# Kernel optimization log

Hardware: AMD Instinct MI355X
Metric: run time of the kernel (lower is better)

## Reference

```python
import jax, jax.numpy as jnp
import numpy as np

N_NODES = 100000
N_EDGES = 1600000
IN_CH = 32
HID = 128
EDGE_DIM = 16
BN_EPS = 1e-5


def setup_inputs() -> dict:
    key = jax.random.key(0)
    ks = jax.random.split(key, 32)
    f32 = jnp.float32

    def w(k, shape, scale):
        return jax.random.normal(k, shape, dtype=f32) * scale

    inp = {
        'x': w(ks[0], (N_NODES, IN_CH), 1.0),
        'edge_index': jax.random.randint(ks[1], (2, N_EDGES), 0, N_NODES, dtype=jnp.int32),
        'edge_attr': w(ks[2], (N_EDGES, EDGE_DIM), 1.0),
        # layer 0: in=32 -> out=128
        'l0_We': w(ks[3], (EDGE_DIM, IN_CH), 0.1),
        'l0_be': jnp.zeros((IN_CH,), f32),
        'l0_W1': w(ks[4], (IN_CH, HID), 0.1),
        'l0_b1': jnp.zeros((HID,), f32),
        'l0_W2': w(ks[5], (HID, HID), 0.1),
        'l0_b2': jnp.zeros((HID,), f32),
        'l0_gamma': jnp.ones((HID,), f32),
        'l0_beta': jnp.zeros((HID,), f32),
        # layer 1: 128 -> 128
        'l1_We': w(ks[6], (EDGE_DIM, HID), 0.1),
        'l1_be': jnp.zeros((HID,), f32),
        'l1_W1': w(ks[7], (HID, HID), 0.1),
        'l1_b1': jnp.zeros((HID,), f32),
        'l1_W2': w(ks[8], (HID, HID), 0.1),
        'l1_b2': jnp.zeros((HID,), f32),
        'l1_gamma': jnp.ones((HID,), f32),
        'l1_beta': jnp.zeros((HID,), f32),
        # head MLP: hidden -> hidden -> 1
        'head_W1': w(ks[9], (HID, HID), 0.1),
        'head_b1': jnp.zeros((HID,), f32),
        'head_W2': w(ks[10], (HID, 1), 0.1),
        'head_b2': jnp.zeros((1,), f32),
    }
    return inp


def _gnblock(x, src, dst, e, We, be, W1, b1, W2, b2, gamma, beta):
    # GINE-style message passing: gather -> edge message -> scatter-sum
    msg = jax.nn.relu(x[src] + e @ We + be)              # [E, d_in]
    agg = jax.ops.segment_sum(msg, dst, num_segments=N_NODES)  # [N, d_in]
    h = x + agg                                          # GIN combine (eps=0)
    h = jax.nn.relu(h @ W1 + b1) @ W2 + b2               # 2-layer MLP
    # batch norm over the node dimension (use_norm=True)
    mu = jnp.mean(h, axis=0)
    var = jnp.var(h, axis=0)
    h = (h - mu) * jax.lax.rsqrt(var + BN_EPS) * gamma + beta
    return jax.nn.relu(h)


def reference(x, edge_index, edge_attr,
              l0_We, l0_be, l0_W1, l0_b1, l0_W2, l0_b2, l0_gamma, l0_beta,
              l1_We, l1_be, l1_W1, l1_b1, l1_W2, l1_b2, l1_gamma, l1_beta,
              head_W1, head_b1, head_W2, head_b2):
    src, dst = edge_index[0], edge_index[1]
    h = _gnblock(x, src, dst, edge_attr,
                 l0_We, l0_be, l0_W1, l0_b1, l0_W2, l0_b2, l0_gamma, l0_beta)
    h = _gnblock(h, src, dst, edge_attr,
                 l1_We, l1_be, l1_W1, l1_b1, l1_W2, l1_b2, l1_gamma, l1_beta)
    # MLPBlock head + sigmoid -> per-node selection probability [N, 1]
    out = jax.nn.relu(h @ head_W1 + head_b1) @ head_W2 + head_b2
    return jax.nn.sigmoid(out)
```

## Files before the change

kernel.cpp:

```cpp
#include <hip/hip_runtime.h>

#define NN 100000
#define NE 1600000
#define TMAX 193760
#define NRANGES 24220

typedef unsigned int uint32;
typedef unsigned long long ull;
typedef __attribute__((ext_vector_type(8))) short bf16x8;
typedef __attribute__((ext_vector_type(4))) float f32x4;

__device__ __forceinline__ unsigned short f2bf(float f) {
  unsigned int u = __float_as_uint(f);
  unsigned int r = (u + 0x7fffu + ((u >> 16) & 1u)) >> 16;
  return (unsigned short)r;
}
__device__ __forceinline__ float bf2f(unsigned short u) {
  return __uint_as_float(((unsigned int)u) << 16);
}
__device__ __forceinline__ unsigned int pack2(float a, float b) {
  return (unsigned int)f2bf(a) | ((unsigned int)f2bf(b) << 16);
}
__device__ __forceinline__ uint32 pack2ru(float a, float b) {
  const uint32 ua = __float_as_uint(a) + 0x8000u;
  const uint32 ub = __float_as_uint(b) + 0x8000u;
  return (ua >> 16) | (ub & 0xffff0000u);
}
__device__ __forceinline__ float row16_sum(float x) {
  x += __int_as_float(__builtin_amdgcn_mov_dpp(__float_as_int(x), 0x128, 0xf, 0xf, false));
  x += __int_as_float(__builtin_amdgcn_mov_dpp(__float_as_int(x), 0x124, 0xf, 0xf, false));
  x += __int_as_float(__builtin_amdgcn_mov_dpp(__float_as_int(x), 0x122, 0xf, 0xf, false));
  x += __int_as_float(__builtin_amdgcn_mov_dpp(__float_as_int(x), 0x121, 0xf, 0xf, false));
  return x;
}

__device__ __forceinline__ void wconv_body(const float* __restrict__ src,
    unsigned short* __restrict__ dst, int K, int N, int b)
{
  const int i = b * 256 + threadIdx.x;
  if (i < K * N) {
    const int n = i / K, k = i - n * K;
    dst[i] = f2bf(src[k * N + n]);
  }
}

__global__ __launch_bounds__(256) void conv_all(
    const float* __restrict__ l0W1, const float* __restrict__ l0W2,
    const float* __restrict__ l1W1, const float* __restrict__ l1W2,
    const float* __restrict__ hW1,  const float* __restrict__ l0We,
    const float* __restrict__ l1We, const float* __restrict__ x,
    unsigned short* __restrict__ W1t0, unsigned short* __restrict__ W2t0,
    unsigned short* __restrict__ W1t1, unsigned short* __restrict__ W2t1,
    unsigned short* __restrict__ hW1t, unsigned short* __restrict__ Wet0,
    unsigned short* __restrict__ Wet1, unsigned short* __restrict__ xb)
{
  int b = blockIdx.x;
  if (b < 16)  { wconv_body(l0W1, W1t0, 32, 128, b); return; }  b -= 16;
  if (b < 64)  { wconv_body(l0W2, W2t0, 128, 128, b); return; } b -= 64;
  if (b < 64)  { wconv_body(l1W1, W1t1, 128, 128, b); return; } b -= 64;
  if (b < 64)  { wconv_body(l1W2, W2t1, 128, 128, b); return; } b -= 64;
  if (b < 64)  { wconv_body(hW1,  hW1t, 128, 128, b); return; } b -= 64;
  if (b < 2)   { wconv_body(l0We, Wet0, 16, 32, b); return; }   b -= 2;
  if (b < 8)   { wconv_body(l1We, Wet1, 16, 128, b); return; }  b -= 8;
  const int i = b * 256 + threadIdx.x;
  if (i * 8 < NN * 32) {
    const float4 a = ((const float4*)x)[i * 2];
    const float4 d = ((const float4*)x)[i * 2 + 1];
    uint4 o;
    o.x = pack2(a.x, a.y); o.y = pack2(a.z, a.w);
    o.z = pack2(d.x, d.y); o.w = pack2(d.z, d.w);
    ((uint4*)xb)[i] = o;
  }
}

__global__ __launch_bounds__(256) void hist_kernel(
    const int* __restrict__ ei, uint32* __restrict__ deg)
{
  const int e = blockIdx.x * 256 + threadIdx.x;
  if (e < NE) atomicAdd(&deg[ei[NE + e]], 1u);
}

__global__ __launch_bounds__(256) void offsets2_kernel(
    const uint32* __restrict__ deg, uint32* __restrict__ toff,
    uint32* __restrict__ eoff, ull* __restrict__ counter)
{
  __shared__ ull s[256];
  __shared__ ull base;
  const int tid = threadIdx.x;
  const int n = blockIdx.x * 256 + tid;
  const uint32 d = (n < NN) ? deg[n] : 0u;
  const uint32 tc = (d + 15u) >> 4;
  const ull v = ((ull)tc << 32) | (ull)d;
  s[tid] = v;
  __syncthreads();
#pragma unroll
  for (int st = 1; st < 256; st <<= 1) {
    ull w = (tid >= st) ? s[tid - st] : 0ull;
    __syncthreads();
    s[tid] += w;
    __syncthreads();
  }
  if (tid == 255) base = atomicAdd(counter, s[255]);
  __syncthreads();
  if (n < NN) {
    const ull t = base + (s[tid] - v);
    toff[n] = (uint32)(t >> 32);
    eoff[n] = (uint32)t;
  }
}

__global__ __launch_bounds__(256) void snode_fill(
    const uint32* __restrict__ toff, const uint32* __restrict__ deg,
    int* __restrict__ snode)
{
  const int n = blockIdx.x * 256 + threadIdx.x;
  if (n < NN) {
    const uint32 t0 = toff[n];
    const uint32 tc = (deg[n] + 15u) >> 4;
    for (uint32 i = 0; i < tc; ++i) snode[t0 + i] = n;
  }
}

__global__ __launch_bounds__(256) void fill_kernel(
    const int* __restrict__ ei, const uint32* __restrict__ eoff,
    uint32* __restrict__ cnt, uint2* __restrict__ esrc2)
{
  const int e = blockIdx.x * 256 + threadIdx.x;
  if (e < NE) {
    const int dst = ei[NE + e];
    const uint32 pos = eoff[dst] + atomicAdd(&cnt[dst], 1u);
    esrc2[pos] = make_uint2((uint32)e, (uint32)ei[e]);
  }
}

template<int D, int NCT>
__global__ __launch_bounds__(256) void flat_agg3(
    const int* __restrict__ snode, const uint32* __restrict__ toff,
    const uint32* __restrict__ eoff, const uint32* __restrict__ deg,
    const uint2* __restrict__ esrc2, const float* __restrict__ ea,
    const unsigned short* __restrict__ hsrc,
    const unsigned short* __restrict__ Wet, const float* __restrict__ be,
    const ull* __restrict__ tot, float* __restrict__ agg)
{
  const int tid = threadIdx.x;
  const int wid = tid >> 6;
  const int lane = tid & 63;
  const int c = lane & 15;
  const int g = lane >> 4;
  constexpr bool HALF = (NCT * 16 != D);
  int range, ch0;
  if (HALF) { range = blockIdx.x * 2 + (wid >> 1); ch0 = (wid & 1) * (NCT * 16); }
  else      { range = blockIdx.x * 4 + wid;        ch0 = 0; }
  const int tile0 = range * 8;
  const uint32 ntile = (uint32)((*tot) >> 32);
  if ((uint32)tile0 >= ntile) return;

  bf16x8 wf[NCT];
#pragma unroll
  for (int ct = 0; ct < NCT; ++ct) {
    const int chA = ch0 + (c >> 2) * (NCT * 4) + ct * 4 + (c & 3);
    uint4 u = make_uint4(0u, 0u, 0u, 0u);
    if (g < 2) u = *(const uint4*)&Wet[chA * 16 + g * 8];
    else if (g == 2) u.x = (0xFE96u << 16) | (uint32)f2bf(be[chA]);
    union { uint4 u4; bf16x8 v; } cv; cv.u4 = u;
    wf[ct] = cv.v;
  }

  int sn8 = -1, pk8 = 0, p_ = 0;
  if (lane < 8) {
    sn8 = snode[tile0 + lane];
    if (sn8 >= 0) {
      const uint32 to = toff[sn8], dg = deg[sn8], eo = eoff[sn8];
      const int k = tile0 + lane - (int)to;
      p_ = (int)eo + k * 16;
      int rv = (int)dg - k * 16; if (rv > 16) rv = 16;
      const int fl = (k == 0 ? 1 : 0) |
                     ((k == (int)((dg + 15u) >> 4) - 1) ? 2 : 0);
      pk8 = (rv << 7) | (fl << 12);
    }
  }
  const int p0base = __shfl(p_, 0);
  if (lane < 8 && sn8 >= 0) pk8 |= (p_ - p0base);

  const uint2 q0 = esrc2[(size_t)p0base + lane];
  const uint2 q1 = esrc2[(size_t)p0base + 64 + lane];

  float acc[NCT][4];
#pragma unroll
  for (int ct = 0; ct < NCT; ++ct) {
    acc[ct][0] = 0.f; acc[ct][1] = 0.f; acc[ct][2] = 0.f; acc[ct][3] = 0.f;
  }
  int openNode = -1; bool openFull = false, openClosed = false;

  auto flushOpen = [&](bool storeOK) {
#pragma unroll
    for (int ct = 0; ct < NCT; ++ct)
#pragma unroll
      for (int j = 0; j < 4; ++j)
        acc[ct][j] = row16_sum(acc[ct][j]);
    float4 sv = make_float4(0.f, 0.f, 0.f, 0.f);
#pragma unroll
    for (int ct = 0; ct < NCT; ++ct)
      if (c == ct)
        sv = make_float4(acc[ct][0], acc[ct][1], acc[ct][2], acc[ct][3]);
    if (c < NCT) {
      float* p = &agg[(size_t)openNode * D + ch0 + g * (NCT * 4) + c * 4];
      if (storeOK) {
        *(float4*)p = sv;
      } else {
        atomicAdd(p + 0, sv.x); atomicAdd(p + 1, sv.y);
        atomicAdd(p + 2, sv.z); atomicAdd(p + 3, sv.w);
      }
    }
  };

  auto issue = [&](int t, float4& E0, float4& E1, uint4& h0, uint4& h1,
                   int& n_, int& mt_) {
    n_ = __shfl(sn8, t);
    mt_ = __shfl(pk8, t);
    const int d0 = mt_ & 127;
    const int rem = (mt_ >> 7) & 31;
    const int idx = d0 + ((c < rem) ? c : 0);
    const int li = idx & 63;
    const uint32 eA = (uint32)__shfl((int)q0.x, li);
    const uint32 eB = (uint32)__shfl((int)q1.x, li);
    const uint32 sA = (uint32)__shfl((int)q0.y, li);
    const uint32 sB = (uint32)__shfl((int)q1.y, li);
    const int e   = (int)((idx & 64) ? eB : eA);
    const int src = (int)((idx & 64) ? sB : sA);
    if (g < 2) {
      E0 = *(const float4*)&ea[(size_t)e * 16 + g * 8];
      E1 = *(const float4*)&ea[(size_t)e * 16 + g * 8 + 4];
    }
    h0 = *(const uint4*)&hsrc[(size_t)src * D + ch0 + g * (NCT * 4)];
    if constexpr (NCT == 4)
      h1 = *(const uint4*)&hsrc[(size_t)src * D + ch0 + g * (NCT * 4) + 8];
  };

  auto compute = [&](const float4 E0, const float4 E1, const uint4 h0,
                     const uint4 h1, const int n, const int mt) {
    if (n < 0) return;
    const int rem = (mt >> 7) & 31;
    const int fl = mt >> 12;
    if (n != openNode) {
      if (openNode >= 0) {
        flushOpen(openFull);
#pragma unroll
        for (int ct = 0; ct < NCT; ++ct) {
          acc[ct][0] = 0.f; acc[ct][1] = 0.f;
          acc[ct][2] = 0.f; acc[ct][3] = 0.f;
        }
      }
      openNode = n; openFull = (fl & 1) != 0; openClosed = false;
    }
    if (fl & 2) openClosed = true;
    bf16x8 afv;
    {
      uint4 u = make_uint4(0u, 0u, 0u, 0u);
      if (g < 2) {
        u.x = pack2ru(E0.x, E0.y); u.y = pack2ru(E0.z, E0.w);
        u.z = pack2ru(E1.x, E1.y); u.w = pack2ru(E1.z, E1.w);
      } else if (g == 2) {
        u.x = (c < rem) ? 0x3f80u : 0x3f803f80u;
      }
      union { uint4 u4; bf16x8 v; } cv; cv.u4 = u; afv = cv.v;
    }
#pragma unroll
    for (int ct = 0; ct < NCT; ++ct) {
      f32x4 pre = __builtin_amdgcn_mfma_f32_16x16x32_bf16(
          wf[ct], afv, (f32x4){0.f, 0.f, 0.f, 0.f}, 0, 0, 0);
#pragma unroll
      for (int j = 0; j < 4; ++j) {
        const int ix = ct * 4 + j;
        const uint4 hu = (ix < 8) ? h0 : h1;
        uint32 wv;
        switch ((ix & 7) >> 1) {
          case 0: wv = hu.x; break;
          case 1: wv = hu.y; break;
          case 2: wv = hu.z; break;
          default: wv = hu.w; break;
        }
        const float hvv = bf2f((unsigned short)((ix & 1) ? (wv >> 16) : (wv & 0xffffu)));
        acc[ct][j] += fmaxf(pre[j] + hvv, 0.f);
      }
    }
  };

  float4 eA0, eA1, eB0, eB1, eC0, eC1;
  uint4 h0A = make_uint4(0,0,0,0), h1A = make_uint4(0,0,0,0);
  uint4 h0B = make_uint4(0,0,0,0), h1B = make_uint4(0,0,0,0);
  uint4 h0C = make_uint4(0,0,0,0), h1C = make_uint4(0,0,0,0);
  int nA = -1, mA = 0, nB = -1, mB = 0, nC = -1, mC = 0;

  issue(0, eA0, eA1, h0A, h1A, nA, mA);
  issue(1, eB0, eB1, h0B, h1B, nB, mB);
  issue(2, eC0, eC1, h0C, h1C, nC, mC);
  compute(eA0, eA1, h0A, h1A, nA, mA); issue(3, eA0, eA1, h0A, h1A, nA, mA);
  compute(eB0, eB1, h0B, h1B, nB, mB); issue(4, eB0, eB1, h0B, h1B, nB, mB);
  compute(eC0, eC1, h0C, h1C, nC, mC); issue(5, eC0, eC1, h0C, h1C, nC, mC);
  compute(eA0, eA1, h0A, h1A, nA, mA); issue(6, eA0, eA1, h0A, h1A, nA, mA);
  compute(eB0, eB1, h0B, h1B, nB, mB); issue(7, eB0, eB1, h0B, h1B, nB, mB);
  compute(eC0, eC1, h0C, h1C, nC, mC);
  compute(eA0, eA1, h0A, h1A, nA, mA);
  compute(eB0, eB1, h0B, h1B, nB, mB);
  if (openNode >= 0) flushOpen(openFull && openClosed);
}

template<int DIN, bool ABF16>
__global__ __launch_bounds__(256) void mlp_mfma(
    const float* __restrict__ a32, const unsigned short* __restrict__ abf,
    const float* __restrict__ agg,
    const unsigned short* __restrict__ W1t, const float* __restrict__ b1,
    const unsigned short* __restrict__ W2t, const float* __restrict__ b2,
    float* __restrict__ outp, float* __restrict__ stats, int nChunks)
{
  constexpr int P1 = (DIN == 128) ? 136 : 40;
  constexpr int KS1 = DIN / 32;
  __shared__ __align__(16) unsigned short hin[64 * P1];
  __shared__ __align__(16) unsigned short tls[64 * 136];
  const int tid = threadIdx.x;
  const int w = tid >> 6;
  const int lane = tid & 63;
  const int c = lane & 15, g = lane >> 4;
  const int cw = w * 32;

  bf16x8 B1[2][KS1], B2[2][4];
#pragma unroll
  for (int ct = 0; ct < 2; ++ct)
#pragma unroll
    for (int kk = 0; kk < KS1; ++kk)
      B1[ct][kk] = *(const bf16x8*)&W1t[(cw + ct * 16 + c) * DIN + kk * 32 + g * 8];
#pragma unroll
  for (int ct = 0; ct < 2; ++ct)
#pragma unroll
    for (int kk = 0; kk < 4; ++kk)
      B2[ct][kk] = *(const bf16x8*)&W2t[(cw + ct * 16 + c) * 128 + kk * 32 + g * 8];
  const float b1c0 = b1[cw + c], b1c1 = b1[cw + 16 + c];
  const float b2c0 = b2[cw + c], b2c1 = b2[cw + 16 + c];
  float lsum0 = 0.f, lsum1 = 0.f, lsq0 = 0.f, lsq1 = 0.f;

  for (int chunk = blockIdx.x; chunk < nChunks; chunk += gridDim.x) {
    const int base = chunk * 64;
    if constexpr (DIN == 128) {
#pragma unroll
      for (int p = 0; p < 4; ++p) {
        const int idx = tid + 256 * p;
        const int n = idx >> 4, k8 = idx & 15;
        const int node = base + n;
        uint4 ov = make_uint4(0u, 0u, 0u, 0u);
        if (node < NN) {
          const float4 g0 = *(const float4*)&agg[node * 128 + k8 * 8];
          const float4 g1 = *(const float4*)&agg[node * 128 + k8 * 8 + 4];
          const uint4 hv = *(const uint4*)&abf[node * 128 + k8 * 8];
          ov.x = pack2(bf2f((unsigned short)(hv.x & 0xffffu)) + g0.x,
                       bf2f((unsigned short)(hv.x >> 16)) + g0.y);
          ov.y = pack2(bf2f((unsigned short)(hv.y & 0xffffu)) + g0.z,
                       bf2f((unsigned short)(hv.y >> 16)) + g0.w);
          ov.z = pack2(bf2f((unsigned short)(hv.z & 0xffffu)) + g1.x,
                       bf2f((unsigned short)(hv.z >> 16)) + g1.y);
          ov.w = pack2(bf2f((unsigned short)(hv.w & 0xffffu)) + g1.z,
                       bf2f((unsigned short)(hv.w >> 16)) + g1.w);
        }
        *(uint4*)&hin[n * P1 + k8 * 8] = ov;
      }
    } else {
      const int n = tid >> 2, k8 = tid & 3;
      const int node = base + n;
      uint4 ov = make_uint4(0u, 0u, 0u, 0u);
      if (node < NN) {
        const float4 x0 = *(const float4*)&a32[node * 32 + k8 * 8];
        const float4 x1 = *(const float4*)&a32[node * 32 + k8 * 8 + 4];
        const float4 g0 = *(const float4*)&agg[node * 32 + k8 * 8];
        const float4 g1 = *(const float4*)&agg[node * 32 + k8 * 8 + 4];
        ov.x = pack2(x0.x + g0.x, x0.y + g0.y);
        ov.y = pack2(x0.z + g0.z, x0.w + g0.w);
        ov.z = pack2(x1.x + g1.x, x1.y + g1.y);
        ov.w = pack2(x1.z + g1.z, x1.w + g1.w);
      }
      *(uint4*)&hin[n * P1 + k8 * 8] = ov;
    }
    __syncthreads();
#pragma unroll
    for (int nt = 0; nt < 4; ++nt) {
      bf16x8 af[KS1];
#pragma unroll
      for (int kk = 0; kk < KS1; ++kk)
        af[kk] = *(const bf16x8*)&hin[(nt * 16 + c) * P1 + kk * 32 + g * 8];
      f32x4 acc0 = {0.f, 0.f, 0.f, 0.f}, acc1 = {0.f, 0.f, 0.f, 0.f};
#pragma unroll
      for (int kk = 0; kk < KS1; ++kk) {
        acc0 = __builtin_amdgcn_mfma_f32_16x16x32_bf16(af[kk], B1[0][kk], acc0, 0, 0, 0);
        acc1 = __builtin_amdgcn_mfma_f32_16x16x32_bf16(af[kk], B1[1][kk], acc1, 0, 0, 0);
      }
#pragma unroll
      for (int j = 0; j < 4; ++j) {
        const int row = nt * 16 + g * 4 + j;
        tls[row * 136 + cw + c]      = f2bf(fmaxf(acc0[j] + b1c0, 0.f));
        tls[row * 136 + cw + 16 + c] = f2bf(fmaxf(acc1[j] + b1c1, 0.f));
      }
    }
    __syncthreads();
#pragma unroll
    for (int nt = 0; nt < 4; ++nt) {
      bf16x8 af[4];
#pragma unroll
      for (int kk = 0; kk < 4; ++kk)
        af[kk] = *(const bf16x8*)&tls[(nt * 16 + c) * 136 + kk * 32 + g * 8];
      f32x4 acc0 = {0.f, 0.f, 0.f, 0.f}, acc1 = {0.f, 0.f, 0.f, 0.f};
#pragma unroll
      for (int kk = 0; kk < 4; ++kk) {
        acc0 = __builtin_amdgcn_mfma_f32_16x16x32_bf16(af[kk], B2[0][kk], acc0, 0, 0, 0);
        acc1 = __builtin_amdgcn_mfma_f32_16x16x32_bf16(af[kk], B2[1][kk], acc1, 0, 0, 0);
      }
#pragma unroll
      for (int j = 0; j < 4; ++j) {
        const int node = base + nt * 16 + g * 4 + j;
        if (node < NN) {
          const float v0 = acc0[j] + b2c0;
          const float v1 = acc1[j] + b2c1;
          outp[node * 128 + cw + c] = v0;
          outp[node * 128 + cw + 16 + c] = v1;
          lsum0 += v0; lsq0 += v0 * v0;
          lsum1 += v1; lsq1 += v1 * v1;
        }
      }
    }
  }
  lsum0 += __shfl_xor(lsum0, 16); lsum0 += __shfl_xor(lsum0, 32);
  lsum1 += __shfl_xor(lsum1, 16); lsum1 += __shfl_xor(lsum1, 32);
  lsq0  += __shfl_xor(lsq0, 16);  lsq0  += __shfl_xor(lsq0, 32);
  lsq1  += __shfl_xor(lsq1, 16);  lsq1  += __shfl_xor(lsq1, 32);
  if (lane < 16) {
    atomicAdd(&stats[cw + lane], lsum0);
    atomicAdd(&stats[cw + 16 + lane], lsum1);
    atomicAdd(&stats[128 + cw + lane], lsq0);
    atomicAdd(&stats[128 + cw + 16 + lane], lsq1);
  }
}

__global__ void bn_finalize(float* __restrict__ stats,
                            const float* __restrict__ gamma,
                            const float* __restrict__ beta)
{
  const int cc = threadIdx.x;
  const float inv_n = 1.0f / (float)NN;
  const float mu = stats[cc] * inv_n;
  float var = stats[128 + cc] * inv_n - mu * mu;
  var = fmaxf(var, 0.f);
  const float rs = rsqrtf(var + 1e-5f);
  const float sc = rs * gamma[cc];
  stats[256 + cc] = sc;
  stats[384 + cc] = beta[cc] - mu * sc;
}

__global__ __launch_bounds__(256) void bn_apply_bf16(
    const float* __restrict__ h, const float* __restrict__ stats,
    unsigned short* __restrict__ hb)
{
  const int idx = blockIdx.x * 256 + threadIdx.x;
  const int c4 = (idx & 31) * 4;
  const float4 sc = *(const float4*)&stats[256 + c4];
  const float4 sh = *(const float4*)&stats[384 + c4];
  const float4 v = ((const float4*)h)[idx];
  const float r0 = fmaxf(fmaf(v.x, sc.x, sh.x), 0.f);
  const float r1 = fmaxf(fmaf(v.y, sc.y, sh.y), 0.f);
  const float r2 = fmaxf(fmaf(v.z, sc.z, sh.z), 0.f);
  const float r3 = fmaxf(fmaf(v.w, sc.w, sh.w), 0.f);
  uint2 o;
  o.x = pack2(r0, r1);
  o.y = pack2(r2, r3);
  ((uint2*)hb)[idx] = o;
}

__global__ __launch_bounds__(256) void head_bn(
    const float* __restrict__ hpre, const float* __restrict__ stats,
    const unsigned short* __restrict__ W1t, const float* __restrict__ b1,
    const float* __restrict__ w2, const float* __restrict__ b2,
    float* __restrict__ out, int nChunks)
{
  __shared__ float pl[4][64];
  const int tid = threadIdx.x;
  const int w = tid >> 6;
  const int lane = tid & 63;
  const int c = lane & 15, g = lane >> 4;
  const int cw = w * 32;

  bf16x8 B1[2][4];
#pragma unroll
  for (int ct = 0; ct < 2; ++ct)
#pragma unroll
    for (int kk = 0; kk < 4; ++kk)
      B1[ct][kk] = *(const bf16x8*)&W1t[(cw + ct * 16 + c) * 128 + kk * 32 + g * 8];
  const float b1c0 = b1[cw + c], b1c1 = b1[cw + 16 + c];
  const float w2c0 = w2[cw + c], w2c1 = w2[cw + 16 + c];
  const float b2v = b2[0];
  float4 scq[4][2], shq[4][2];
#pragma unroll
  for (int kk = 0; kk < 4; ++kk) {
    const int cb = kk * 32 + g * 8;
    scq[kk][0] = *(const float4*)&stats[256 + cb];
    scq[kk][1] = *(const float4*)&stats[256 + cb + 4];
    shq[kk][0] = *(const float4*)&stats[384 + cb];
    shq[kk][1] = *(const float4*)&stats[384 + cb + 4];
  }

  for (int chunk = blockIdx.x; chunk < nChunks; chunk += gridDim.x) {
    const int base = chunk * 64;
    float p[4][4];
#pragma unroll
    for (int nt = 0; nt < 4; ++nt) {
      const int node = base + nt * 16 + c;
      bf16x8 af[4];
#pragma unroll
      for (int kk = 0; kk < 4; ++kk) {
        uint4 u = make_uint4(0u, 0u, 0u, 0u);
        if (node < NN) {
          const float4 v0 = *(const float4*)&hpre[(size_t)node * 128 + kk * 32 + g * 8];
          const float4 v1 = *(const float4*)&hpre[(size_t)node * 128 + kk * 32 + g * 8 + 4];
          const float4 s0 = scq[kk][0], s1 = scq[kk][1];
          const float4 h0 = shq[kk][0], h1 = shq[kk][1];
          u.x = pack2(fmaxf(fmaf(v0.x, s0.x, h0.x), 0.f),
                      fmaxf(fmaf(v0.y, s0.y, h0.y), 0.f));
          u.y = pack2(fmaxf(fmaf(v0.z, s0.z, h0.z), 0.f),
                      fmaxf(fmaf(v0.w, s0.w, h0.w), 0.f));
          u.z = pack2(fmaxf(fmaf(v1.x, s1.x, h1.x), 0.f),
                      fmaxf(fmaf(v1.y, s1.y, h1.y), 0.f));
          u.w = pack2(fmaxf(fmaf(v1.z, s1.z, h1.z), 0.f),
                      fmaxf(fmaf(v1.w, s1.w, h1.w), 0.f));
        }
        union { uint4 u4; bf16x8 v; } cv; cv.u4 = u;
        af[kk] = cv.v;
      }
      f32x4 acc0 = {0.f, 0.f, 0.f, 0.f}, acc1 = {0.f, 0.f, 0.f, 0.f};
#pragma unroll
      for (int kk = 0; kk < 4; ++kk) {
        acc0 = __builtin_amdgcn_mfma_f32_16x16x32_bf16(af[kk], B1[0][kk], acc0, 0, 0, 0);
        acc1 = __builtin_amdgcn_mfma_f32_16x16x32_bf16(af[kk], B1[1][kk], acc1, 0, 0, 0);
      }
#pragma unroll
      for (int j = 0; j < 4; ++j)
        p[nt][j] = fmaxf(acc0[j] + b1c0, 0.f) * w2c0 +
                   fmaxf(acc1[j] + b1c1, 0.f) * w2c1;
    }
#pragma unroll
    for (int dd = 1; dd <= 8; dd <<= 1)
#pragma unroll
      for (int nt = 0; nt < 4; ++nt)
#pragma unroll
        for (int j = 0; j < 4; ++j)
          p[nt][j] += __shfl_xor(p[nt][j], dd);
    if (c == 0) {
#pragma unroll
      for (int nt = 0; nt < 4; ++nt)
#pragma unroll
        for (int j = 0; j < 4; ++j)
          pl[w][nt * 16 + g * 4 + j] = p[nt][j];
    }
    __syncthreads();
    if (tid < 64) {
      const int node = base + tid;
      if (node < NN) {
        const float s = pl[0][tid] + pl[1][tid] + pl[2][tid] + pl[3][tid] + b2v;
        out[node] = 1.f / (1.f + expf(-s));
      }
    }
    __syncthreads();
  }
}

extern "C" void kernel_launch(void* const* d_in, const int* in_sizes, int n_in,
                              void* d_out, int out_size, void* d_ws, size_t ws_size,
                              hipStream_t stream)
{
  const float* x    = (const float*)d_in[0];
  const int*   ei   = (const int*)  d_in[1];
  const float* ea   = (const float*)d_in[2];
  const float* l0We = (const float*)d_in[3];
  const float* l0be = (const float*)d_in[4];
  const float* l0W1 = (const float*)d_in[5];
  const float* l0b1 = (const float*)d_in[6];
  const float* l0W2 = (const float*)d_in[7];
  const float* l0b2 = (const float*)d_in[8];
  const float* l0g  = (const float*)d_in[9];
  const float* l0bt = (const float*)d_in[10];
  const float* l1We = (const float*)d_in[11];
  const float* l1be = (const float*)d_in[12];
  const float* l1W1 = (const float*)d_in[13];
  const float* l1b1 = (const float*)d_in[14];
  const float* l1W2 = (const float*)d_in[15];
  const float* l1b2 = (const float*)d_in[16];
  const float* l1g  = (const float*)d_in[17];
  const float* l1bt = (const float*)d_in[18];
  const float* hW1  = (const float*)d_in[19];
  const float* hb1  = (const float*)d_in[20];
  const float* hW2  = (const float*)d_in[21];
  const float* hb2  = (const float*)d_in[22];
  float* out = (float*)d_out;

  float*  A    = (float*)d_ws;
  float*  AGG  = A + (size_t)NN * 128;
  unsigned short* hb = (unsigned short*)(AGG + (size_t)NN * 128);
  unsigned short* xb = hb + (size_t)NN * 128;
  uint32* deg     = (uint32*)(xb + (size_t)NN * 32);
  uint32* cnt     = deg + NN;
  uint32* toff    = cnt + NN;
  uint32* eoff    = toff + NN;
  ull*    counter = (ull*)(eoff + NN);
  int*    snode   = (int*)(counter + 2);
  uint2*  esrc2   = (uint2*)(snode + TMAX);
  float*  st0     = (float*)(esrc2 + NE + 128);
  float*  st1     = st0 + 512;
  unsigned short* W1t0 = (unsigned short*)(st1 + 512);
  unsigned short* W2t0 = W1t0 + 4096;
  unsigned short* W1t1 = W2t0 + 16384;
  unsigned short* W2t1 = W1t1 + 16384;
  unsigned short* hW1t = W2t1 + 16384;
  unsigned short* Wet0 = hW1t + 16384;
  unsigned short* Wet1 = Wet0 + 512;

  const size_t needed = (size_t)((char*)(Wet1 + 2048) - (char*)d_ws);
  if (ws_size < needed) return;

  hipMemsetAsync(deg, 0, (size_t)2 * NN * 4, stream);
  hipMemsetAsync(counter, 0, 16, stream);
  hipMemsetAsync(snode, 0xFF, (size_t)TMAX * 4, stream);
  hipMemsetAsync(st0, 0, 4096, stream);
  hipMemsetAsync(AGG, 0, (size_t)NN * 32 * 4, stream);

  const int nChunks = (NN + 63) / 64;
  const int eBlocks = (NE + 255) / 256;

  conv_all<<<16 + 64 * 4 + 2 + 8 + 1563, 256, 0, stream>>>(
      l0W1, l0W2, l1W1, l1W2, hW1, l0We, l1We, x,
      W1t0, W2t0, W1t1, W2t1, hW1t, Wet0, Wet1, xb);

  hist_kernel<<<eBlocks, 256, 0, stream>>>(ei, deg);
  offsets2_kernel<<<(NN + 255) / 256, 256, 0, stream>>>(deg, toff, eoff, counter);
  snode_fill<<<(NN + 255) / 256, 256, 0, stream>>>(toff, deg, snode);
  fill_kernel<<<eBlocks, 256, 0, stream>>>(ei, eoff, cnt, esrc2);

  flat_agg3<32, 2><<<NRANGES / 4, 256, 0, stream>>>(
      snode, toff, eoff, deg, esrc2, ea, xb, Wet0, l0be, counter, AGG);
  mlp_mfma<32, false><<<782, 256, 0, stream>>>(x, (const unsigned short*)nullptr,
      AGG, W1t0, l0b1, W2t0, l0b2, A, st0, nChunks);
  hipMemsetAsync(AGG, 0, (size_t)NN * 128 * 4, stream);
  bn_finalize<<<1, 128, 0, stream>>>(st0, l0g, l0bt);
  bn_apply_bf16<<<(NN * 32) / 256, 256, 0, stream>>>(A, st0, hb);

  flat_agg3<128, 4><<<NRANGES / 2, 256, 0, stream>>>(
      snode, toff, eoff, deg, esrc2, ea, hb, Wet1, l1be, counter, AGG);
  mlp_mfma<128, true><<<782, 256, 0, stream>>>((const float*)nullptr, hb,
      AGG, W1t1, l1b1, W2t1, l1b2, A, st1, nChunks);
  bn_finalize<<<1, 128, 0, stream>>>(st1, l1g, l1bt);

  head_bn<<<782, 256, 0, stream>>>(A, st1, hW1t, hb1, hW2, hb2, out, nChunks);
}
```

Measured before the change: 589.5 us.

## Cache bf16 edge attributes in CSR order, fold h into MFMA accumulator

Layer 0 aggregation now writes the bf16-packed edge attributes into a workspace buffer laid out in destination-sorted CSR order. Layer 1 then reads that buffer contiguously instead of gathering fp32 edge_attr through the edge-id indirection. This halves bytes and makes the access sequential. Separately, the gathered node feature is passed as the MFMA C operand so the add happens inside the matrix instruction. The costs are an extra 51 MB workspace, extra stores in layer 0, and a dependence on p0base being consistent across both layers.

```diff
diff --git a/kernel.cpp b/kernel.cpp
--- a/kernel.cpp
+++ b/kernel.cpp
@@ -133,11 +133,12 @@
   }
 }
 
-template<int D, int NCT>
-__global__ __launch_bounds__(256) void flat_agg3(
+template<int D, int NCT, bool GEA>
+__global__ __launch_bounds__(256) void flat_agg4(
     const int* __restrict__ snode, const uint32* __restrict__ toff,
     const uint32* __restrict__ eoff, const uint32* __restrict__ deg,
     const uint2* __restrict__ esrc2, const float* __restrict__ ea,
+    unsigned short* __restrict__ eabc,
     const unsigned short* __restrict__ hsrc,
     const unsigned short* __restrict__ Wet, const float* __restrict__ be,
     const ull* __restrict__ tot, float* __restrict__ agg)
@@ -214,31 +215,35 @@
     }
   };
 
-  auto issue = [&](int t, float4& E0, float4& E1, uint4& h0, uint4& h1,
-                   int& n_, int& mt_) {
+  auto issue = [&](int t, float4& E0, float4& E1, uint4& afu,
+                   uint4& h0, uint4& h1, int& n_, int& mt_) {
     n_ = __shfl(sn8, t);
     mt_ = __shfl(pk8, t);
     const int d0 = mt_ & 127;
     const int rem = (mt_ >> 7) & 31;
     const int idx = d0 + ((c < rem) ? c : 0);
     const int li = idx & 63;
-    const uint32 eA = (uint32)__shfl((int)q0.x, li);
-    const uint32 eB = (uint32)__shfl((int)q1.x, li);
     const uint32 sA = (uint32)__shfl((int)q0.y, li);
     const uint32 sB = (uint32)__shfl((int)q1.y, li);
-    const int e   = (int)((idx & 64) ? eB : eA);
     const int src = (int)((idx & 64) ? sB : sA);
-    if (g < 2) {
-      E0 = *(const float4*)&ea[(size_t)e * 16 + g * 8];
-      E1 = *(const float4*)&ea[(size_t)e * 16 + g * 8 + 4];
+    if constexpr (GEA) {
+      const uint32 eA = (uint32)__shfl((int)q0.x, li);
+      const uint32 eB = (uint32)__shfl((int)q1.x, li);
+      const int e = (int)((idx & 64) ? eB : eA);
+      if (g < 2) {
+        E0 = *(const float4*)&ea[(size_t)e * 16 + g * 8];
+        E1 = *(const float4*)&ea[(size_t)e * 16 + g * 8 + 4];
+      }
+    } else {
+      if (g < 2) afu = *(const uint4*)&eabc[((size_t)p0base + idx) * 16 + g * 8];
     }
     h0 = *(const uint4*)&hsrc[(size_t)src * D + ch0 + g * (NCT * 4)];
     if constexpr (NCT == 4)
       h1 = *(const uint4*)&hsrc[(size_t)src * D + ch0 + g * (NCT * 4) + 8];
   };
 
-  auto compute = [&](const float4 E0, const float4 E1, const uint4 h0,
-                     const uint4 h1, const int n, const int mt) {
+  auto compute = [&](const float4 E0, const float4 E1, uint4 afu,
+                     const uint4 h0, const uint4 h1, const int n, const int mt) {
     if (n < 0) return;
     const int rem = (mt >> 7) & 31;
     const int fl = mt >> 12;
@@ -254,55 +259,65 @@
       openNode = n; openFull = (fl & 1) != 0; openClosed = false;
     }
     if (fl & 2) openClosed = true;
+    if constexpr (GEA) {
+      afu.x = pack2ru(E0.x, E0.y); afu.y = pack2ru(E0.z, E0.w);
+      afu.z = pack2ru(E1.x, E1.y); afu.w = pack2ru(E1.z, E1.w);
+      if (g < 2) {
+        const int d0 = mt & 127;
+        const int idx = d0 + ((c < rem) ? c : 0);
+        *(uint4*)&eabc[((size_t)p0base + idx) * 16 + g * 8] = afu;
+      }
+    }
     bf16x8 afv;
     {
       uint4 u = make_uint4(0u, 0u, 0u, 0u);
-      if (g < 2) {
-        u.x = pack2ru(E0.x, E0.y); u.y = pack2ru(E0.z, E0.w);
-        u.z = pack2ru(E1.x, E1.y); u.w = pack2ru(E1.z, E1.w);
-      } else if (g == 2) {
-        u.x = (c < rem) ? 0x3f80u : 0x3f803f80u;
-      }
+      if (g < 2) u = afu;
+      else if (g == 2) u.x = (c < rem) ? 0x3f80u : 0x3f803f80u;
       union { uint4 u4; bf16x8 v; } cv; cv.u4 = u; afv = cv.v;
     }
 #pragma unroll
     for (int ct = 0; ct < NCT; ++ct) {
+      uint32 w0, w1;
+      if constexpr (NCT == 4) {
+        const uint4 hu = (ct < 2) ? h0 : h1;
+        w0 = (ct & 1) ? hu.z : hu.x;
+        w1 = (ct & 1) ? hu.w : hu.y;
+      } else {
+        w0 = (ct & 1) ? h0.z : h0.x;
+        w1 = (ct & 1) ? h0.w : h0.y;
+      }
+      f32x4 hC;
+      hC[0] = bf2f((unsigned short)(w0 & 0xffffu));
+      hC[1] = bf2f((unsigned short)(w0 >> 16));
+      hC[2] = bf2f((unsigned short)(w1 & 0xffffu));
+      hC[3] = bf2f((unsigned short)(w1 >> 16));
       f32x4 pre = __builtin_amdgcn_mfma_f32_16x16x32_bf16(
-          wf[ct], afv, (f32x4){0.f, 0.f, 0.f, 0.f}, 0, 0, 0);
-#pragma unroll
-      for (int j = 0; j < 4; ++j) {
-        const int ix = ct * 4 + j;
-        const uint4 hu = (ix < 8) ? h0 : h1;
-        uint32 wv;
-        switch ((ix & 7) >> 1) {
-          case 0: wv = hu.x; break;
-          case 1: wv = hu.y; break;
-          case 2: wv = hu.z; break;
-          default: wv = hu.w; break;
-        }
-        const float hvv = bf2f((unsigned short)((ix & 1) ? (wv >> 16) : (wv & 0xffffu)));
-        acc[ct][j] += fmaxf(pre[j] + hvv, 0.f);
-      }
+          wf[ct], afv, hC, 0, 0, 0);
+      acc[ct][0] += fmaxf(pre[0], 0.f);
+      acc[ct][1] += fmaxf(pre[1], 0.f);
+      acc[ct][2] += fmaxf(pre[2], 0.f);
+      acc[ct][3] += fmaxf(pre[3], 0.f);
     }
   };
 
   float4 eA0, eA1, eB0, eB1, eC0, eC1;
+  uint4 aA = make_uint4(0,0,0,0), aB = make_uint4(0,0,0,0), aC = make_uint4(0,0,0,0);
   uint4 h0A = make_uint4(0,0,0,0), h1A = make_uint4(0,0,0,0);
   uint4 h0B = make_uint4(0,0,0,0), h1B = make_uint4(0,0,0,0);
   uint4 h0C = make_uint4(0,0,0,0), h1C = make_uint4(0,0,0,0);
   int nA = -1, mA = 0, nB = -1, mB = 0, nC = -1, mC = 0;
 
-  issue(0, eA0, eA1, h0A, h1A, nA, mA);
-  issue(1, eB0, eB1, h0B, h1B, nB, mB);
-  issue(2, eC0, eC1, h0C, h1C, nC, mC);
-  compute(eA0, eA1, h0A, h1A, nA, mA); issue(3, eA0, eA1, h0A, h1A, nA, mA);
-  compute(eB0, eB1, h0B, h1B, nB, mB); issue(4, eB0, eB1, h0B, h1B, nB, mB);
-  compute(eC0, eC1, h0C, h1C, nC, mC); issue(5, eC0, eC1, h0C, h1C, nC, mC);
-  compute(eA0, eA1, h0A, h1A, nA, mA); issue(6, eA0, eA1, h0A, h1A, nA, mA);
-  compute(eB0, eB1, h0B, h1B, nB, mB); issue(7, eB0, eB1, h0B, h1B, nB, mB);
-  compute(eC0, eC1, h0C, h1C, nC, mC);
-  compute(eA0, eA1, h0A, h1A, nA, mA);
-  compute(eB0, eB1, h0B, h1B, nB, mB);
+  issue(0, eA0, eA1, aA, h0A, h1A, nA, mA);
+  issue(1, eB0, eB1, aB, h0B, h1B, nB, mB);
+  issue(2, eC0, eC1, aC, h0C, h1C, nC, mC);
+  compute(eA0, eA1, aA, h0A, h1A, nA, mA); issue(3, eA0, eA1, aA, h0A, h1A, nA, mA);
+  compute(eB0, eB1, aB, h0B, h1B, nB, mB); issue(4, eB0, eB1, aB, h0B, h1B, nB, mB);
+  compute(eC0, eC1, aC, h0C, h1C, nC, mC); issue(5, eC0, eC1, aC, h0C, h1C, nC, mC);
+  compute(eA0, eA1, aA, h0A, h1A, nA, mA); issue(6, eA0, eA1, aA, h0A, h1A, nA, mA);
+  compute(eB0, eB1, aB, h0B, h1B, nB, mB); issue(7, eB0, eB1, aB, h0B, h1B, nB, mB);
+  compute(eC0, eC1, aC, h0C, h1C, nC, mC);
+  compute(eA0, eA1, aA, h0A, h1A, nA, mA);
+  compute(eB0, eB1, aB, h0B, h1B, nB, mB);
   if (openNode >= 0) flushOpen(openFull && openClosed);
 }
 
@@ -617,8 +632,9 @@
   unsigned short* hW1t = W2t1 + 16384;
   unsigned short* Wet0 = hW1t + 16384;
   unsigned short* Wet1 = Wet0 + 512;
-
-  const size_t needed = (size_t)((char*)(Wet1 + 2048) - (char*)d_ws);
+  unsigned short* eabc = Wet1 + 2048;
+
+  const size_t needed = (size_t)((char*)(eabc + (size_t)NE * 16) - (char*)d_ws);
   if (ws_size < needed) return;
 
   hipMemsetAsync(deg, 0, (size_t)2 * NN * 4, stream);
@@ -639,16 +655,16 @@
   snode_fill<<<(NN + 255) / 256, 256, 0, stream>>>(toff, deg, snode);
   fill_kernel<<<eBlocks, 256, 0, stream>>>(ei, eoff, cnt, esrc2);
 
-  flat_agg3<32, 2><<<NRANGES / 4, 256, 0, stream>>>(
-      snode, toff, eoff, deg, esrc2, ea, xb, Wet0, l0be, counter, AGG);
+  flat_agg4<32, 2, true><<<NRANGES / 4, 256, 0, stream>>>(
+      snode, toff, eoff, deg, esrc2, ea, eabc, xb, Wet0, l0be, counter, AGG);
   mlp_mfma<32, false><<<782, 256, 0, stream>>>(x, (const unsigned short*)nullptr,
       AGG, W1t0, l0b1, W2t0, l0b2, A, st0, nChunks);
   hipMemsetAsync(AGG, 0, (size_t)NN * 128 * 4, stream);
   bn_finalize<<<1, 128, 0, stream>>>(st0, l0g, l0bt);
   bn_apply_bf16<<<(NN * 32) / 256, 256, 0, stream>>>(A, st0, hb);
 
-  flat_agg3<128, 4><<<NRANGES / 2, 256, 0, stream>>>(
-      snode, toff, eoff, deg, esrc2, ea, hb, Wet1, l1be, counter, AGG);
+  flat_agg4<128, 4, false><<<NRANGES / 2, 256, 0, stream>>>(
+      snode, toff, eoff, deg, esrc2, ea, eabc, hb, Wet1, l1be, counter, AGG);
   mlp_mfma<128, true><<<782, 256, 0, stream>>>((const float*)nullptr, hb,
       AGG, W1t1, l1b1, W2t1, l1b2, A, st1, nChunks);
   bn_finalize<<<1, 128, 0, stream>>>(st1, l1g, l1bt);
```

After: 561.2 us. 1.05x faster.
